# Kernel optimization log

Measured on AMD Instinct MI355X. Metric: run time of the kernel, lower is better.

Reference implementation:

```python
import jax, jax.numpy as jnp
import numpy as np

GRAPH_ALPHA = 3.0
HOP_ALPHA = 0.05
TOP_K = 30


def conv1x1(x, W, b):
    # x: [B,C,N,T], W: [O,C] -> [B,O,N,T]
    return jnp.einsum('bcnt,oc->bont', x, W) + b[None, :, None, None]


def tconv(x, W, b):
    # temporal conv along T, kernel (1,3), 'same' padding. W: [O,I,1,3]
    y = jax.lax.conv_general_dilated(x, W, (1, 1), ((0, 0), (1, 1)),
                                     dimension_numbers=('NCHW', 'OIHW', 'NCHW'))
    return y + b[None, :, None, None]


def mixprop(x, adj, W, b):
    # 1-hop mix-prop graph diffusion (gcn_depth=1, hopalpha=0.05)
    n = adj.shape[0]
    A = adj + jnp.eye(n, dtype=adj.dtype)
    A = A / A.sum(axis=1, keepdims=True)
    h = HOP_ALPHA * x + (1.0 - HOP_ALPHA) * jnp.einsum('bcvt,vw->bcwt', x, A)
    return conv1x1(jnp.concatenate([x, h], axis=1), W, b)


def st_block(x, adj, tf_w, tf_b, tg_w, tg_b, g1_w, g1_b, g2_w, g2_b,
             end_w, end_b, out_w, out_b):
    h = jnp.tanh(tconv(x, tf_w, tf_b)) * jax.nn.sigmoid(tconv(x, tg_w, tg_b))
    h = mixprop(h, adj, g1_w, g1_b) + mixprop(h, adj.T, g2_w, g2_b)
    h = jax.nn.relu(conv1x1(h, end_w, end_b))
    return conv1x1(h, out_w, out_b)


def build_adj(idx, emb1, emb2, l1_w, l1_b, l2_w, l2_b):
    e1, e2 = emb1[idx], emb2[idx]
    n1 = jnp.tanh(GRAPH_ALPHA * (e1 @ l1_w.T + l1_b))
    n2 = jnp.tanh(GRAPH_ALPHA * (e2 @ l2_w.T + l2_b))
    a = n1 @ n2.T - n2 @ n1.T
    adj = jax.nn.relu(jnp.tanh(GRAPH_ALPHA * a))
    _, top_idx = jax.lax.top_k(adj, TOP_K)
    rows = jnp.arange(adj.shape[0])[:, None]
    mask = jnp.zeros_like(adj).at[rows, top_idx].set(1.0)
    return adj * mask


def setup_inputs() -> dict:
    B, T, N, D = 16, 128, 1024, 64
    ks = jax.random.split(jax.random.key(0), 24)
    def w(i, shape):
        return jax.random.normal(ks[i], shape, dtype=jnp.float32) * 0.1
    z = lambda *s: jnp.zeros(s, jnp.float32)
    return {
        'x': jax.random.normal(ks[0], (B, T, N), dtype=jnp.float32),
        'idx': jnp.arange(N, dtype=jnp.int32),
        'emb1': w(1, (N, D)), 'emb2': w(2, (N, D)),
        'lin1_w': w(3, (D, D)), 'lin1_b': z(D),
        'lin2_w': w(4, (D, D)), 'lin2_b': z(D),
        'w_start': w(5, (16, 1)), 'b_start': z(16),
        'enc_tf_w': w(6, (16, 16, 1, 3)), 'enc_tf_b': z(16),
        'enc_tg_w': w(7, (16, 16, 1, 3)), 'enc_tg_b': z(16),
        'enc_g1_w': w(8, (16, 32)), 'enc_g1_b': z(16),
        'enc_g2_w': w(9, (16, 32)), 'enc_g2_b': z(16),
        'enc_end_w': w(10, (32, 16)), 'enc_end_b': z(32),
        'enc_out_w': w(11, (64, 32)), 'enc_out_b': z(64),
        'dec_tf_w': w(12, (64, 64, 1, 3)), 'dec_tf_b': z(64),
        'dec_tg_w': w(13, (64, 64, 1, 3)), 'dec_tg_b': z(64),
        'dec_g1_w': w(14, (64, 128)), 'dec_g1_b': z(64),
        'dec_g2_w': w(15, (64, 128)), 'dec_g2_b': z(64),
        'dec_end_w': w(16, (32, 64)), 'dec_end_b': z(32),
        'dec_out_w': w(17, (16, 32)), 'dec_out_b': z(16),
        'w_end': w(18, (1, 16)), 'b_end': z(1),
    }


def reference(x, idx, emb1, emb2, lin1_w, lin1_b, lin2_w, lin2_b,
              w_start, b_start,
              enc_tf_w, enc_tf_b, enc_tg_w, enc_tg_b, enc_g1_w, enc_g1_b,
              enc_g2_w, enc_g2_b, enc_end_w, enc_end_b, enc_out_w, enc_out_b,
              dec_tf_w, dec_tf_b, dec_tg_w, dec_tg_b, dec_g1_w, dec_g1_b,
              dec_g2_w, dec_g2_b, dec_end_w, dec_end_b, dec_out_w, dec_out_b,
              w_end, b_end):
    adj = build_adj(idx, emb1, emb2, lin1_w, lin1_b, lin2_w, lin2_b)
    h = jnp.transpose(x, (0, 2, 1))[:, None]  # [B,1,N,T]
    h = conv1x1(h, w_start, b_start)          # [B,16,N,T]
    z = st_block(h, adj, enc_tf_w, enc_tf_b, enc_tg_w, enc_tg_b,
                 enc_g1_w, enc_g1_b, enc_g2_w, enc_g2_b,
                 enc_end_w, enc_end_b, enc_out_w, enc_out_b)  # [B,64,N,T]
    y = st_block(z, adj, dec_tf_w, dec_tf_b, dec_tg_w, dec_tg_b,
                 dec_g1_w, dec_g1_b, dec_g2_w, dec_g2_b,
                 dec_end_w, dec_end_b, dec_out_w, dec_out_b)  # [B,16,N,T]
    y = conv1x1(y, w_end, b_end)               # [B,1,N,T]
    return jnp.transpose(y[:, 0], (0, 2, 1))   # [B,T,N]
```

## Files before the change

### kernel.cpp

```cpp
#include <hip/hip_runtime.h>
#include <math.h>

#define NN   1024
#define TTL  128
#define NTP  131072
#define TOPK 30

#define OEGTF_T 0
#define OEGTF_C 48
#define OEGTF_B 96
#define OEGTG_T 112
#define OEGTG_C 160
#define OEGTG_B 208
#define OEE0    224
#define OEE1    736
#define OEE2    1248
#define OEEB    1760
#define OEOUT_W 1792
#define OEOUT_B 3840
#define ODTF_B  16192
#define ODTG_B  28544
#define ODEB    34752
#define OWC     34784
#define OBC     34816
#define ODEALL  59456
#define ODTW2   65600
#define OCF     77888
#define OCG     78080
#define WTOT    78272


__global__ void k_prep_weights(
    const float* __restrict__ w_start, const float* __restrict__ b_start,
    const float* __restrict__ etf_w, const float* __restrict__ etf_b,
    const float* __restrict__ etg_w, const float* __restrict__ etg_b,
    const float* __restrict__ eg1_w, const float* __restrict__ eg1_b,
    const float* __restrict__ eg2_w, const float* __restrict__ eg2_b,
    const float* __restrict__ eend_w, const float* __restrict__ eend_b,
    const float* __restrict__ eout_w, const float* __restrict__ eout_b,
    const float* __restrict__ dtf_w, const float* __restrict__ dtf_b,
    const float* __restrict__ dtg_w, const float* __restrict__ dtg_b,
    const float* __restrict__ dg1_w, const float* __restrict__ dg1_b,
    const float* __restrict__ dg2_w, const float* __restrict__ dg2_b,
    const float* __restrict__ dend_w, const float* __restrict__ dend_b,
    const float* __restrict__ dout_w, const float* __restrict__ dout_b,
    const float* __restrict__ w_end, const float* __restrict__ b_end,
    float* __restrict__ W)
{
    int tid = blockIdx.x*blockDim.x + threadIdx.x;
    int nthr = gridDim.x*blockDim.x;
    for (int id=tid; id<96; id+=nthr){
        int which = id/48; int r = id%48; int o = r/3, k = r%3;
        const float* w = which ? etg_w : etf_w;
        double t=0.0, c=0.0;
        for (int i=0;i<16;i++){
            double wv = (double)w[(o*16+i)*3+k];
            t += wv*(double)w_start[i];
            c += wv*(double)b_start[i];
        }
        W[(which?OEGTG_T:OEGTF_T)+o*3+k] = (float)t;
        W[(which?OEGTG_C:OEGTF_C)+o*3+k] = (float)c;
    }
    for (int i=tid;i<16;i+=nthr){
        W[OEGTF_B+i] = etf_b[i];
        W[OEGTG_B+i] = etg_b[i];
    }
    for (int id=tid; id<512; id+=nthr){
        int i = id>>5, o2 = id&31;
        double s0=0.0, s1=0.0, s2=0.0;
        for (int o=0;o<16;o++){
            double m0 = (double)eg1_w[o*32+i] + (double)eg2_w[o*32+i]
                      + 0.05*((double)eg1_w[o*32+16+i] + (double)eg2_w[o*32+16+i]);
            double m1 = 0.95*(double)eg1_w[o*32+16+i];
            double m2 = 0.95*(double)eg2_w[o*32+16+i];
            double ew = (double)eend_w[o2*16+o];
            s0 += ew*m0; s1 += ew*m1; s2 += ew*m2;
        }
        W[OEE0+i*32+o2]=(float)s0; W[OEE1+i*32+o2]=(float)s1; W[OEE2+i*32+o2]=(float)s2;
    }
    for (int o2=tid; o2<32; o2+=nthr){
        double s = (double)eend_b[o2];
        for (int o=0;o<16;o++) s += (double)eend_w[o2*16+o]*((double)eg1_b[o]+(double)eg2_b[o]);
        W[OEEB+o2] = (float)s;
    }
    for (int i=tid;i<64;i+=nthr){
        W[ODTF_B+i]=dtf_b[i]; W[ODTG_B+i]=dtg_b[i];
    }
    for (int id=tid; id<12288; id+=nthr){
        int oc = id/3072; int rem = id%3072; int j = rem/96; int q = rem%96;
        const float* w = (q<48) ? dtf_w : dtg_w;
        int q2 = (q<48) ? q : q-48;
        int o = q2/3, k = q2%3;
        double s = 0.0;
        for (int i=0;i<64;i++)
            s += (double)w[((oc*16+o)*64+i)*3+k]*(double)eout_w[i*32+j];
        W[ODTW2+id] = (float)s;
    }
    for (int id=tid; id<384; id+=nthr){
        int which = id/192; int r = id%192;
        int oc = r/48; int q = r%48; int o = q/3, k = q%3;
        const float* w = which ? dtg_w : dtf_w;
        double s = 0.0;
        for (int i=0;i<64;i++)
            s += (double)w[((oc*16+o)*64+i)*3+k]*(double)eout_b[i];
        W[(which?OCG:OCF) + oc*48 + o*3 + k] = (float)s;
    }
    for (int id=tid; id<6144; id+=nthr){
        int i = id/96, j = id%96;
        double s = 0.0;
        if (j < 32){
            int o2 = j;
            for (int o=0;o<64;o++){
                double m1 = 0.95*(double)dg1_w[o*128+64+i];
                s += (double)dend_w[o2*64+o]*m1;
            }
        } else if (j < 64){
            int o2 = j-32;
            for (int o=0;o<64;o++){
                double m2 = 0.95*(double)dg2_w[o*128+64+i];
                s += (double)dend_w[o2*64+o]*m2;
            }
        } else {
            int o2 = j-64;
            for (int o=0;o<64;o++){
                double m0 = (double)dg1_w[o*128+i] + (double)dg2_w[o*128+i]
                          + 0.05*((double)dg1_w[o*128+64+i] + (double)dg2_w[o*128+64+i]);
                s += (double)dend_w[o2*64+o]*m0;
            }
        }
        W[ODEALL+id] = (float)s;
    }
    for (int o2=tid; o2<32; o2+=nthr){
        double s = (double)dend_b[o2];
        for (int o=0;o<64;o++) s += (double)dend_w[o2*64+o]*((double)dg1_b[o]+(double)dg2_b[o]);
        W[ODEB+o2] = (float)s;
        double wc = 0.0;
        for (int o3=0;o3<16;o3++) wc += (double)w_end[o3]*(double)dout_w[o3*32+o2];
        W[OWC+o2] = (float)wc;
    }
    if (tid==0){
        double bc = (double)b_end[0];
        for (int o3=0;o3<16;o3++) bc += (double)w_end[o3]*(double)dout_b[o3];
        W[OBC] = (float)bc;
    }
}

__global__ void k_emb(const int* __restrict__ idxp,
                      const float* __restrict__ emb1, const float* __restrict__ emb2,
                      const float* __restrict__ l1w, const float* __restrict__ l1b,
                      const float* __restrict__ l2w, const float* __restrict__ l2b,
                      double* __restrict__ n1, double* __restrict__ n2)
{
    int id = blockIdx.x*blockDim.x + threadIdx.x;
    int i = id>>6, d = id&63;
    int ii = idxp[i];
    double a1 = (double)l1b[d], a2 = (double)l2b[d];
    for (int k=0;k<64;k++){
        a1 += (double)emb1[ii*64+k]*(double)l1w[d*64+k];
        a2 += (double)emb2[ii*64+k]*(double)l2w[d*64+k];
    }
    n1[id] = tanh(3.0*a1);
    n2[id] = tanh(3.0*a2);
}

__global__ __launch_bounds__(64) void k_topk(
    const double* __restrict__ n1, const double* __restrict__ n2,
    int* __restrict__ topc, double* __restrict__ topv,
    double* __restrict__ rs1, double* __restrict__ colsum)
{
    __shared__ double arow[NN];
    __shared__ double sn1[64], sn2[64];
    int i = blockIdx.x, lane = threadIdx.x;
    sn1[lane] = n1[i*64+lane];
    sn2[lane] = n2[i*64+lane];
    __syncthreads();
    for (int jb=0;jb<16;jb++){
        int j = jb*64 + lane;
        const double* p2 = n2 + (long)j*64;
        const double* p1 = n1 + (long)j*64;
        double d1v=0.0, d2v=0.0;
        for (int d=0;d<64;d++){ d1v += sn1[d]*p2[d]; d2v += sn2[d]*p1[d]; }
        double a = tanh(3.0*(d1v - d2v));
        arow[j] = a>0.0 ? a : 0.0;
    }
    __syncthreads();
    double lv = -2.0; int lj = 1<<30;
    for (int jb=0;jb<16;jb++){
        int j = jb*64+lane;
        double v = arow[j];
        if (v>lv || (v==lv && j<lj)){ lv=v; lj=j; }
    }
    double rsum = 0.0;
    for (int r=0;r<TOPK;r++){
        double bv = lv; int bj = lj;
        for (int off=32; off>=1; off>>=1){
            double ov = __shfl_xor(bv, off, 64);
            int    oj = __shfl_xor(bj, off, 64);
            if (ov>bv || (ov==bv && oj<bj)){ bv=ov; bj=oj; }
        }
        if (lane == (bj & 63)){
            arow[bj] = -2.0;
            lv = -2.0; lj = 1<<30;
            for (int jb=0;jb<16;jb++){
                int j = jb*64+lane;
                double v = arow[j];
                if (v>lv || (v==lv && j<lj)){ lv=v; lj=j; }
            }
        }
        if (lane == 0){
            topc[i*TOPK+r] = bj;
            topv[i*TOPK+r] = bv;
            if (bv > 0.0) atomicAdd(&colsum[bj], bv);
        }
        rsum += (bv > 0.0 ? bv : 0.0);
    }
    if (lane == 0) rs1[i] = 1.0 + rsum;
}

__global__ void k_csc(const int* __restrict__ topc, const double* __restrict__ topv,
                      const double* __restrict__ rs1,
                      int* __restrict__ ccount, int* __restrict__ cidx, float* __restrict__ cw)
{
    int w = blockIdx.x*blockDim.x + threadIdx.x;
    if (w >= NN) return;
    double rv = rs1[w];
    for (int r=0;r<TOPK;r++){
        double v = topv[w*TOPK+r];
        if (v > 0.0){
            int col = topc[w*TOPK+r];
            int pos = atomicAdd(&ccount[col], 1);
            cidx[(long)col*NN+pos] = w;
            cw  [(long)col*NN+pos] = (float)(v / rv);
        }
    }
}

__global__ void k_pad(int* __restrict__ ccount, int* __restrict__ cidx, float* __restrict__ cw)
{
    int col = blockIdx.x*blockDim.x + threadIdx.x;
    if (col >= NN) return;
    int cnt = ccount[col];
    int padded = (cnt + 7) & ~7;
    for (int e = cnt; e < padded; e++){
        cidx[(long)col*NN + e] = 0;
        cw  [(long)col*NN + e] = 0.0f;
    }
    ccount[col] = padded;
}

__global__ void k_post1(const double* __restrict__ colsum, const double* __restrict__ rs1,
                        double* __restrict__ rs2, float* __restrict__ d1, float* __restrict__ d2)
{
    int v = blockIdx.x*blockDim.x + threadIdx.x;
    if (v >= NN) return;
    double r2 = 1.0 + colsum[v];
    rs2[v] = r2;
    d2[v] = (float)(1.0/r2);
    d1[v] = (float)(1.0/rs1[v]);
}

__global__ void k_post2(const int* __restrict__ topc, const double* __restrict__ topv,
                        const double* __restrict__ rs2,
                        int* __restrict__ topc2, float* __restrict__ ew2b)
{
    int e = blockIdx.x*blockDim.x + threadIdx.x;
    if (e >= NN*32) return;
    int w = e>>5, r = e&31;
    if (r < TOPK){
        double v = topv[w*TOPK+r];
        int c = topc[w*TOPK+r];
        topc2[e] = (v > 0.0) ? c : 0;
        ew2b[e]  = (v > 0.0) ? (float)(v / rs2[c]) : 0.0f;
    } else {
        topc2[e] = 0;
        ew2b[e]  = 0.0f;
    }
}


__global__ __launch_bounds__(256) void k_enc_gg(const float* __restrict__ x,
    float* __restrict__ eg, float* __restrict__ es1, float* __restrict__ es2,
    const float* __restrict__ Wt,
    const int* __restrict__ ccount, const int* __restrict__ cidx, const float* __restrict__ cw,
    const int* __restrict__ topc2, const float* __restrict__ ew2b,
    const float* __restrict__ d1, const float* __restrict__ d2,
    long S, int b0)
{
    __shared__ float4 lA[NN];
    __shared__ float4 lB[NN];
    int tid = threadIdx.x, c = blockIdx.y, cb = blockIdx.z, t0 = blockIdx.x*8;
    float ft[3], fc[3], gt[3], gcc[3];
    #pragma unroll
    for (int k=0;k<3;k++){
        ft[k]=Wt[OEGTF_T+c*3+k]; fc[k]=Wt[OEGTF_C+c*3+k];
        gt[k]=Wt[OEGTG_T+c*3+k]; gcc[k]=Wt[OEGTG_C+c*3+k];
    }
    float fb = Wt[OEGTF_B+c], gb = Wt[OEGTG_B+c];
    const float* xb = x + (long)(b0+cb)*NTP + (long)t0*NN;
    long base = (long)c*S + (long)cb*NTP + (long)t0*NN;
    bool hl0 = (t0>0), hr7 = (t0+8<TTL);
    for (int q=0;q<4;q++){
        int v = q*256 + tid;
        float xr[10];
        xr[0] = hl0 ? xb[v-NN] : 0.0f;
        #pragma unroll
        for (int k=0;k<8;k++) xr[k+1] = xb[v+(long)k*NN];
        xr[9] = hr7 ? xb[v+(long)8*NN] : 0.0f;
        float gg[8];
        #pragma unroll
        for (int k=0;k<8;k++){
            float atf = fb + ft[1]*xr[k+1] + fc[1];
            float atg = gb + gt[1]*xr[k+1] + gcc[1];
            bool hL = (k>0) || hl0;
            bool hR = (k<7) || hr7;
            if (hL){ atf += ft[0]*xr[k] + fc[0]; atg += gt[0]*xr[k] + gcc[0]; }
            if (hR){ atf += ft[2]*xr[k+2] + fc[2]; atg += gt[2]*xr[k+2] + gcc[2]; }
            gg[k] = tanhf(atf)/(1.0f+expf(-atg));
            eg[base + (long)k*NN + v] = gg[k];
        }
        lA[v] = make_float4(gg[0],gg[1],gg[2],gg[3]);
        lB[v] = make_float4(gg[4],gg[5],gg[6],gg[7]);
    }
    __syncthreads();
    for (int wb=0;wb<4;wb++){
        int w = wb*256 + tid;
        float4 ga = lA[w], gbv = lB[w];
        float dv = d1[w];
        float a0=ga.x*dv, a1=ga.y*dv, a2=ga.z*dv, a3=ga.w*dv;
        float a4=gbv.x*dv, a5=gbv.y*dv, a6=gbv.z*dv, a7=gbv.w*dv;
        int cnt = ccount[w];
        const int4*   ci4 = (const int4*)  (cidx + (long)w*NN);
        const float4* cw4 = (const float4*)(cw   + (long)w*NN);
        for (int e=0; e<cnt; e+=4){
            int4 ia = ci4[e>>2];
            float4 wa = cw4[e>>2];
            float4 s, u;
            s = lA[ia.x]; u = lB[ia.x];
            a0 += wa.x*s.x; a1 += wa.x*s.y; a2 += wa.x*s.z; a3 += wa.x*s.w;
            a4 += wa.x*u.x; a5 += wa.x*u.y; a6 += wa.x*u.z; a7 += wa.x*u.w;
            s = lA[ia.y]; u = lB[ia.y];
            a0 += wa.y*s.x; a1 += wa.y*s.y; a2 += wa.y*s.z; a3 += wa.y*s.w;
            a4 += wa.y*u.x; a5 += wa.y*u.y; a6 += wa.y*u.z; a7 += wa.y*u.w;
            s = lA[ia.z]; u = lB[ia.z];
            a0 += wa.z*s.x; a1 += wa.z*s.y; a2 += wa.z*s.z; a3 += wa.z*s.w;
            a4 += wa.z*u.x; a5 += wa.z*u.y; a6 += wa.z*u.z; a7 += wa.z*u.w;
            s = lA[ia.w]; u = lB[ia.w];
            a0 += wa.w*s.x; a1 += wa.w*s.y; a2 += wa.w*s.z; a3 += wa.w*s.w;
            a4 += wa.w*u.x; a5 += wa.w*u.y; a6 += wa.w*u.z; a7 += wa.w*u.w;
        }
        es1[base+w]=a0; es1[base+NN+w]=a1; es1[base+2*NN+w]=a2; es1[base+3*NN+w]=a3;
        es1[base+4*NN+w]=a4; es1[base+5*NN+w]=a5; es1[base+6*NN+w]=a6; es1[base+7*NN+w]=a7;
        float dw = d2[w];
        a0=ga.x*dw; a1=ga.y*dw; a2=ga.z*dw; a3=ga.w*dw;
        a4=gbv.x*dw; a5=gbv.y*dw; a6=gbv.z*dw; a7=gbv.w*dw;
        const int4*   tc4 = (const int4*)  (topc2 + w*32);
        const float4* e24 = (const float4*)(ew2b  + w*32);
        #pragma unroll
        for (int r=0;r<8;r++){
            int4 ic = tc4[r]; float4 wv = e24[r];
            float4 s, u;
            s = lA[ic.x]; u = lB[ic.x];
            a0 += wv.x*s.x; a1 += wv.x*s.y; a2 += wv.x*s.z; a3 += wv.x*s.w;
            a4 += wv.x*u.x; a5 += wv.x*u.y; a6 += wv.x*u.z; a7 += wv.x*u.w;
            s = lA[ic.y]; u = lB[ic.y];
            a0 += wv.y*s.x; a1 += wv.y*s.y; a2 += wv.y*s.z; a3 += wv.y*s.w;
            a4 += wv.y*u.x; a5 += wv.y*u.y; a6 += wv.y*u.z; a7 += wv.y*u.w;
            s = lA[ic.z]; u = lB[ic.z];
            a0 += wv.z*s.x; a1 += wv.z*s.y; a2 += wv.z*s.z; a3 += wv.z*s.w;
            a4 += wv.z*u.x; a5 += wv.z*u.y; a6 += wv.z*u.z; a7 += wv.z*u.w;
            s = lA[ic.w]; u = lB[ic.w];
            a0 += wv.w*s.x; a1 += wv.w*s.y; a2 += wv.w*s.z; a3 += wv.w*s.w;
            a4 += wv.w*u.x; a5 += wv.w*u.y; a6 += wv.w*u.z; a7 += wv.w*u.w;
        }
        es2[base+w]=a0; es2[base+NN+w]=a1; es2[base+2*NN+w]=a2; es2[base+3*NN+w]=a3;
        es2[base+4*NN+w]=a4; es2[base+5*NN+w]=a5; es2[base+6*NN+w]=a6; es2[base+7*NN+w]=a7;
    }
}

__global__ __launch_bounds__(256) void k_enc_tail(const float* __restrict__ Bp,
    float* __restrict__ E32, const float* __restrict__ Wt, long S)
{
    long p = (long)blockIdx.x*256 + threadIdx.x;
    float e[32];
    #pragma unroll
    for (int o2=0;o2<32;o2++) e[o2] = Wt[OEEB+o2];
    for (int i=0;i<16;i++){
        float a = Bp[(long)i*S+p], b = Bp[(long)(16+i)*S+p], c = Bp[(long)(32+i)*S+p];
        const float* w0 = Wt+OEE0+i*32;
        const float* w1 = Wt+OEE1+i*32;
        const float* w2 = Wt+OEE2+i*32;
        #pragma unroll
        for (int o2=0;o2<32;o2++) e[o2] += w0[o2]*a + w1[o2]*b + w2[o2]*c;
    }
    #pragma unroll
    for (int o2=0;o2<32;o2++){
        float v = e[o2];
        E32[(long)o2*S+p] = v>0.0f ? v : 0.0f;
    }
}

__global__ __launch_bounds__(256) void k_dec_gate(const float* __restrict__ E32,
    float* __restrict__ g, const float* __restrict__ Wt, long S)
{
    int oc = blockIdx.y;
    long pos = (long)blockIdx.x*256 + threadIdx.x;
    int t = (int)((pos>>10) & (TTL-1));
    bool hasL = (t>0), hasR = (t<TTL-1);
    float af[16], ag[16];
    #pragma unroll
    for (int o=0;o<16;o++){
        float bf = Wt[ODTF_B+oc*16+o] + Wt[OCF+oc*48+o*3+1];
        float bg = Wt[ODTG_B+oc*16+o] + Wt[OCG+oc*48+o*3+1];
        if (hasL){ bf += Wt[OCF+oc*48+o*3];   bg += Wt[OCG+oc*48+o*3]; }
        if (hasR){ bf += Wt[OCF+oc*48+o*3+2]; bg += Wt[OCG+oc*48+o*3+2]; }
        af[o]=bf; ag[o]=bg;
    }
    #pragma unroll 1
    for (int j=0;j<32;j++){
        const float* xp = E32 + (long)j*S + pos;
        float xc = xp[0];
        float xl = hasL ? xp[-NN] : 0.0f;
        float xr = hasR ? xp[NN]  : 0.0f;
        const float* wfg = Wt + ODTW2 + (long)(oc*32+j)*96;
        #pragma unroll
        for (int o=0;o<16;o++){
            af[o] += wfg[o*3]*xl + wfg[o*3+1]*xc + wfg[o*3+2]*xr;
            ag[o] += wfg[48+o*3]*xl + wfg[48+o*3+1]*xc + wfg[48+o*3+2]*xr;
        }
    }
    #pragma unroll
    for (int o=0;o<16;o++){
        g[(long)(oc*16+o)*S + pos] = tanhf(af[o])/(1.0f+expf(-ag[o]));
    }
}

__global__ __launch_bounds__(256) void k_dec_conv(const float* __restrict__ g,
    float* __restrict__ Cp, float* __restrict__ P0p,
    const float* __restrict__ Wt, long S)
{
    long p = (long)blockIdx.x*256 + threadIdx.x;
    int jc = blockIdx.y;
    if (jc == 0){
        float a1[32], a2[32];
        #pragma unroll
        for (int jj=0;jj<32;jj++){ a1[jj]=0.0f; a2[jj]=0.0f; }
        #pragma unroll 1
        for (int i=0;i<64;i++){
            float gv = g[(long)i*S+p];
            const float* wr = Wt + ODEALL + i*96;
            #pragma unroll
            for (int jj=0;jj<32;jj++){ a1[jj] += wr[jj]*gv; a2[jj] += wr[32+jj]*gv; }
        }
        #pragma unroll
        for (int jj=0;jj<32;jj++){
            Cp[(long)jj*S+p] = a1[jj];
            Cp[(long)(32+jj)*S+p] = a2[jj];
        }
    } else {
        float a0[32];
        #pragma unroll
        for (int jj=0;jj<32;jj++) a0[jj] = Wt[ODEB+jj];
        #pragma unroll 1
        for (int i=0;i<64;i++){
            float gv = g[(long)i*S+p];
            const float* wr = Wt + ODEALL + i*96 + 64;
            #pragma unroll
            for (int jj=0;jj<32;jj++) a0[jj] += wr[jj]*gv;
        }
        #pragma unroll
        for (int jj=0;jj<32;jj++) P0p[(long)jj*S+p] = a0[jj];
    }
}

__global__ __launch_bounds__(256) void k_graph32f(const float* __restrict__ P1,
    const float* __restrict__ P2, const float* __restrict__ P0,
    float* __restrict__ part,
    const int* __restrict__ ccount, const int* __restrict__ cidx, const float* __restrict__ cw,
    const int* __restrict__ topc2, const float* __restrict__ ew2b,
    const float* __restrict__ d1, const float* __restrict__ d2,
    const float* __restrict__ Wt, long S)
{
    __shared__ float4 lA[NN];
    __shared__ float4 lB[NN];
    int tid = threadIdx.x;
    int grp = blockIdx.y, cb = blockIdx.z, t0 = blockIdx.x*8;
    long tbase = (long)cb*NTP + (long)t0*NN;
    float res[4][8];
    #pragma unroll
    for (int wb=0;wb<4;wb++){
        #pragma unroll
        for (int k=0;k<8;k++) res[wb][k]=0.0f;
    }
    float q1[4][8];
    for (int c4=0;c4<4;c4++){
        int ch = grp*4 + c4;
        long base = (long)ch*S + tbase;
        if (c4) __syncthreads();
        const float* s1 = P1 + base;
        for (int q=0;q<4;q++){
            int v = q*256 + tid;
            lA[v] = make_float4(s1[v], s1[v+NN], s1[v+2*NN], s1[v+3*NN]);
            lB[v] = make_float4(s1[v+4*NN], s1[v+5*NN], s1[v+6*NN], s1[v+7*NN]);
        }
        __syncthreads();
        for (int wb=0;wb<4;wb++){
            int w = wb*256 + tid;
            float4 ga = lA[w], gbv = lB[w];
            float dv = d1[w];
            float a0=ga.x*dv, a1=ga.y*dv, a2=ga.z*dv, a3=ga.w*dv;
            float a4=gbv.x*dv, a5=gbv.y*dv, a6=gbv.z*dv, a7=gbv.w*dv;
            int cnt = ccount[w];
            const int4*   ci4 = (const int4*)  (cidx + (long)w*NN);
            const float4* cw4 = (const float4*)(cw   + (long)w*NN);
            for (int e=0; e<cnt; e+=4){
                int4 ia = ci4[e>>2];
                float4 wa = cw4[e>>2];
                float4 s, u;
                s = lA[ia.x]; u = lB[ia.x];
                a0 += wa.x*s.x; a1 += wa.x*s.y; a2 += wa.x*s.z; a3 += wa.x*s.w;
                a4 += wa.x*u.x; a5 += wa.x*u.y; a6 += wa.x*u.z; a7 += wa.x*u.w;
                s = lA[ia.y]; u = lB[ia.y];
                a0 += wa.y*s.x; a1 += wa.y*s.y; a2 += wa.y*s.z; a3 += wa.y*s.w;
                a4 += wa.y*u.x; a5 += wa.y*u.y; a6 += wa.y*u.z; a7 += wa.y*u.w;
                s = lA[ia.z]; u = lB[ia.z];
                a0 += wa.z*s.x; a1 += wa.z*s.y; a2 += wa.z*s.z; a3 += wa.z*s.w;
                a4 += wa.z*u.x; a5 += wa.z*u.y; a6 += wa.z*u.z; a7 += wa.z*u.w;
                s = lA[ia.w]; u = lB[ia.w];
                a0 += wa.w*s.x; a1 += wa.w*s.y; a2 += wa.w*s.z; a3 += wa.w*s.w;
                a4 += wa.w*u.x; a5 += wa.w*u.y; a6 += wa.w*u.z; a7 += wa.w*u.w;
            }
            q1[wb][0]=a0; q1[wb][1]=a1; q1[wb][2]=a2; q1[wb][3]=a3;
            q1[wb][4]=a4; q1[wb][5]=a5; q1[wb][6]=a6; q1[wb][7]=a7;
        }
        __syncthreads();
        const float* s2 = P2 + base;
        for (int q=0;q<4;q++){
            int v = q*256 + tid;
            lA[v] = make_float4(s2[v], s2[v+NN], s2[v+2*NN], s2[v+3*NN]);
            lB[v] = make_float4(s2[v+4*NN], s2[v+5*NN], s2[v+6*NN], s2[v+7*NN]);
        }
        __syncthreads();
        float wc = Wt[OWC+ch];
        const float* p0 = P0 + base;
        for (int wb=0;wb<4;wb++){
            int w = wb*256 + tid;
            float4 ga = lA[w], gbv = lB[w];
            float dw = d2[w];
            float a0=ga.x*dw, a1=ga.y*dw, a2=ga.z*dw, a3=ga.w*dw;
            float a4=gbv.x*dw, a5=gbv.y*dw, a6=gbv.z*dw, a7=gbv.w*dw;
            const int4*   tc4 = (const int4*)  (topc2 + w*32);
            const float4* e24 = (const float4*)(ew2b  + w*32);
            #pragma unroll
            for (int r=0;r<8;r++){
                int4 ic = tc4[r]; float4 wv = e24[r];
                float4 s, u;
                s = lA[ic.x]; u = lB[ic.x];
                a0 += wv.x*s.x; a1 += wv.x*s.y; a2 += wv.x*s.z; a3 += wv.x*s.w;
                a4 += wv.x*u.x; a5 += wv.x*u.y; a6 += wv.x*u.z; a7 += wv.x*u.w;
                s = lA[ic.y]; u = lB[ic.y];
                a0 += wv.y*s.x; a1 += wv.y*s.y; a2 += wv.y*s.z; a3 += wv.y*s.w;
                a4 += wv.y*u.x; a5 += wv.y*u.y; a6 += wv.y*u.z; a7 += wv.y*u.w;
                s = lA[ic.z]; u = lB[ic.z];
                a0 += wv.z*s.x; a1 += wv.z*s.y; a2 += wv.z*s.z; a3 += wv.z*s.w;
                a4 += wv.z*u.x; a5 += wv.z*u.y; a6 += wv.z*u.z; a7 += wv.z*u.w;
                s = lA[ic.w]; u = lB[ic.w];
                a0 += wv.w*s.x; a1 += wv.w*s.y; a2 += wv.w*s.z; a3 += wv.w*s.w;
                a4 += wv.w*u.x; a5 += wv.w*u.y; a6 += wv.w*u.z; a7 += wv.w*u.w;
            }
            float e0,e1,e2,e3,e4,e5,e6,e7;
            e0 = p0[w]      + q1[wb][0] + a0;
            e1 = p0[NN+w]   + q1[wb][1] + a1;
            e2 = p0[2*NN+w] + q1[wb][2] + a2;
            e3 = p0[3*NN+w] + q1[wb][3] + a3;
            e4 = p0[4*NN+w] + q1[wb][4] + a4;
            e5 = p0[5*NN+w] + q1[wb][5] + a5;
            e6 = p0[6*NN+w] + q1[wb][6] + a6;
            e7 = p0[7*NN+w] + q1[wb][7] + a7;
            e0 = e0>0.0f?e0:0.0f; e1 = e1>0.0f?e1:0.0f;
            e2 = e2>0.0f?e2:0.0f; e3 = e3>0.0f?e3:0.0f;
            e4 = e4>0.0f?e4:0.0f; e5 = e5>0.0f?e5:0.0f;
            e6 = e6>0.0f?e6:0.0f; e7 = e7>0.0f?e7:0.0f;
            res[wb][0] += wc*e0; res[wb][1] += wc*e1;
            res[wb][2] += wc*e2; res[wb][3] += wc*e3;
            res[wb][4] += wc*e4; res[wb][5] += wc*e5;
            res[wb][6] += wc*e6; res[wb][7] += wc*e7;
        }
    }
    long pb = (long)grp*S + tbase;
    for (int wb=0;wb<4;wb++){
        int w = wb*256 + tid;
        #pragma unroll
        for (int k=0;k<8;k++) part[pb+(long)k*NN+w] = res[wb][k];
    }
}

__global__ __launch_bounds__(256) void k_comb(const float* __restrict__ part,
    const float* __restrict__ Wt, float* __restrict__ out, long S, int b0)
{
    long p = (long)blockIdx.x*256 + threadIdx.x;
    float r = Wt[OBC];
    #pragma unroll
    for (int gp=0; gp<8; gp++) r += part[(long)gp*S+p];
    out[(long)b0*NTP + p] = r;
}


extern "C" void kernel_launch(void* const* d_in, const int* in_sizes, int n_in,
                              void* d_out, int out_size, void* d_ws, size_t ws_size,
                              hipStream_t stream)
{
    const float* x      = (const float*)d_in[0];
    const int*   idx    = (const int*)  d_in[1];
    const float* emb1   = (const float*)d_in[2];
    const float* emb2   = (const float*)d_in[3];
    const float* lin1_w = (const float*)d_in[4];
    const float* lin1_b = (const float*)d_in[5];
    const float* lin2_w = (const float*)d_in[6];
    const float* lin2_b = (const float*)d_in[7];
    const float* w_start= (const float*)d_in[8];
    const float* b_start= (const float*)d_in[9];
    const float* etf_w  = (const float*)d_in[10];
    const float* etf_b  = (const float*)d_in[11];
    const float* etg_w  = (const float*)d_in[12];
    const float* etg_b  = (const float*)d_in[13];
    const float* eg1_w  = (const float*)d_in[14];
    const float* eg1_b  = (const float*)d_in[15];
    const float* eg2_w  = (const float*)d_in[16];
    const float* eg2_b  = (const float*)d_in[17];
    const float* eend_w = (const float*)d_in[18];
    const float* eend_b = (const float*)d_in[19];
    const float* eout_w = (const float*)d_in[20];
    const float* eout_b = (const float*)d_in[21];
    const float* dtf_w  = (const float*)d_in[22];
    const float* dtf_b  = (const float*)d_in[23];
    const float* dtg_w  = (const float*)d_in[24];
    const float* dtg_b  = (const float*)d_in[25];
    const float* dg1_w  = (const float*)d_in[26];
    const float* dg1_b  = (const float*)d_in[27];
    const float* dg2_w  = (const float*)d_in[28];
    const float* dg2_b  = (const float*)d_in[29];
    const float* dend_w = (const float*)d_in[30];
    const float* dend_b = (const float*)d_in[31];
    const float* dout_w = (const float*)d_in[32];
    const float* dout_b = (const float*)d_in[33];
    const float* w_end  = (const float*)d_in[34];
    const float* b_end  = (const float*)d_in[35];
    float* out = (float*)d_out;

    char* basep = (char*)d_ws;
    size_t cur = 0;
    auto alloc = [&](size_t bytes)->void* {
        void* p = basep + cur;
        cur = (cur + bytes + 511) & ~(size_t)511;
        return p;
    };
    float*  W     = (float*) alloc(WTOT*sizeof(float));
    double* n1    = (double*)alloc(65536*sizeof(double));
    double* n2    = (double*)alloc(65536*sizeof(double));
    double* topv  = (double*)alloc((size_t)NN*TOPK*sizeof(double));
    int*    topc  = (int*)   alloc((size_t)NN*TOPK*sizeof(int));
    double* rs1   = (double*)alloc(NN*sizeof(double));
    double* rs2   = (double*)alloc(NN*sizeof(double));
    double* colsum= (double*)alloc(NN*sizeof(double));
    float*  d1a   = (float*) alloc(NN*sizeof(float));
    float*  d2a   = (float*) alloc(NN*sizeof(float));
    int*    topc2 = (int*)   alloc((size_t)NN*32*sizeof(int));
    float*  ew2b  = (float*) alloc((size_t)NN*32*sizeof(float));
    int*    ccount= (int*)   alloc(NN*sizeof(int));
    int*    cidx  = (int*)   alloc((size_t)NN*NN*sizeof(int));
    float*  cw    = (float*) alloc((size_t)NN*NN*sizeof(float));

    size_t perb = (size_t)176 * NTP * sizeof(float);
    int CB = 1;
    for (int c = 16; c >= 1; c >>= 1){
        if (cur + perb*(size_t)c <= ws_size){ CB = c; break; }
    }
    long S = (long)CB * NTP;
    float* A = (float*)alloc((size_t)64*S*sizeof(float));
    float* B = (float*)alloc((size_t)48*S*sizeof(float));
    float* C = (float*)alloc((size_t)64*S*sizeof(float));

    (void)hipMemsetAsync(colsum, 0, NN*sizeof(double), stream);
    (void)hipMemsetAsync(ccount, 0, NN*sizeof(int), stream);

    k_prep_weights<<<32,256,0,stream>>>(
        w_start,b_start, etf_w,etf_b, etg_w,etg_b, eg1_w,eg1_b, eg2_w,eg2_b,
        eend_w,eend_b, eout_w,eout_b, dtf_w,dtf_b, dtg_w,dtg_b, dg1_w,dg1_b,
        dg2_w,dg2_b, dend_w,dend_b, dout_w,dout_b, w_end,b_end, W);
    k_emb<<<256,256,0,stream>>>(idx, emb1, emb2, lin1_w, lin1_b, lin2_w, lin2_b, n1, n2);
    k_topk<<<NN,64,0,stream>>>(n1, n2, topc, topv, rs1, colsum);
    k_csc<<<4,256,0,stream>>>(topc, topv, rs1, ccount, cidx, cw);
    k_pad<<<4,256,0,stream>>>(ccount, cidx, cw);
    k_post1<<<4,256,0,stream>>>(colsum, rs1, rs2, d1a, d2a);
    k_post2<<<(NN*32+255)/256,256,0,stream>>>(topc, topv, rs2, topc2, ew2b);

    int nch = 16 / CB;
    for (int ch=0; ch<nch; ch++){
        int b0 = ch*CB;
        k_enc_gg<<<dim3(16,16,CB),256,0,stream>>>(x, B, B+(long)16*S, B+(long)32*S, W,
            ccount,cidx,cw, topc2,ew2b, d1a,d2a, S, b0);
        k_enc_tail<<<512*CB,256,0,stream>>>(B, A, W, S);
        k_dec_gate<<<dim3(512*CB,4),256,0,stream>>>(A, C, W, S);
        k_dec_conv<<<dim3(512*CB,2),256,0,stream>>>(C, A, B, W, S);
        k_graph32f<<<dim3(16,8,CB),256,0,stream>>>(A, A+(long)32*S, B, C,
            ccount,cidx,cw, topc2,ew2b, d1a,d2a, W, S);
        k_comb<<<512*CB,256,0,stream>>>(C, W, out, S, b0);
    }
    (void)in_sizes; (void)n_in; (void)out_size;
}
```

Before: 3.625 ms.

## Fuse decoder gate and conv kernels via LDS; transpose embeddings for top-k

Merges the decoder gated temporal conv and the following 1x1 projection kernels into one kernel. The 64-channel gate output now stays in a 64KB shared-memory tile instead of round-tripping through global memory, and buffer roles are reshuffled to match. Separately, the embedding kernel also writes transposed copies of n1/n2 so the top-k dot products read coalesced columns. The trade-off is less parallelism, since each block now does all four gate output groups serially, and the large LDS footprint limits occupancy.

```diff
diff --git a/kernel.cpp b/kernel.cpp
--- a/kernel.cpp
+++ b/kernel.cpp
@@ -149,7 +149,8 @@
                       const float* __restrict__ emb1, const float* __restrict__ emb2,
                       const float* __restrict__ l1w, const float* __restrict__ l1b,
                       const float* __restrict__ l2w, const float* __restrict__ l2b,
-                      double* __restrict__ n1, double* __restrict__ n2)
+                      double* __restrict__ n1, double* __restrict__ n2,
+                      double* __restrict__ n1T, double* __restrict__ n2T)
 {
     int id = blockIdx.x*blockDim.x + threadIdx.x;
     int i = id>>6, d = id&63;
@@ -159,12 +160,14 @@
         a1 += (double)emb1[ii*64+k]*(double)l1w[d*64+k];
         a2 += (double)emb2[ii*64+k]*(double)l2w[d*64+k];
     }
-    n1[id] = tanh(3.0*a1);
-    n2[id] = tanh(3.0*a2);
+    double v1 = tanh(3.0*a1), v2 = tanh(3.0*a2);
+    n1[id] = v1;            n2[id] = v2;
+    n1T[d*NN+i] = v1;       n2T[d*NN+i] = v2;
 }
 
 __global__ __launch_bounds__(64) void k_topk(
     const double* __restrict__ n1, const double* __restrict__ n2,
+    const double* __restrict__ n1T, const double* __restrict__ n2T,
     int* __restrict__ topc, double* __restrict__ topv,
     double* __restrict__ rs1, double* __restrict__ colsum)
 {
@@ -176,10 +179,11 @@
     __syncthreads();
     for (int jb=0;jb<16;jb++){
         int j = jb*64 + lane;
-        const double* p2 = n2 + (long)j*64;
-        const double* p1 = n1 + (long)j*64;
         double d1v=0.0, d2v=0.0;
-        for (int d=0;d<64;d++){ d1v += sn1[d]*p2[d]; d2v += sn2[d]*p1[d]; }
+        for (int d=0;d<64;d++){
+            d1v += sn1[d]*n2T[d*NN+j];
+            d2v += sn2[d]*n1T[d*NN+j];
+        }
         double a = tanh(3.0*(d1v - d2v));
         arow[j] = a>0.0 ? a : 0.0;
     }
@@ -399,70 +403,66 @@
     }
 }
 
-__global__ __launch_bounds__(256) void k_dec_gate(const float* __restrict__ E32,
-    float* __restrict__ g, const float* __restrict__ Wt, long S)
-{
-    int oc = blockIdx.y;
-    long pos = (long)blockIdx.x*256 + threadIdx.x;
-    int t = (int)((pos>>10) & (TTL-1));
+__global__ __launch_bounds__(256) void k_dec_fused(const float* __restrict__ E32,
+    float* __restrict__ P12, float* __restrict__ P0p,
+    const float* __restrict__ Wt, long S)
+{
+    __shared__ float gl[64*256];
+    int tid = threadIdx.x;
+    long p = (long)blockIdx.x*256 + tid;
+    int t = (int)((p>>10) & (TTL-1));
     bool hasL = (t>0), hasR = (t<TTL-1);
-    float af[16], ag[16];
-    #pragma unroll
-    for (int o=0;o<16;o++){
-        float bf = Wt[ODTF_B+oc*16+o] + Wt[OCF+oc*48+o*3+1];
-        float bg = Wt[ODTG_B+oc*16+o] + Wt[OCG+oc*48+o*3+1];
-        if (hasL){ bf += Wt[OCF+oc*48+o*3];   bg += Wt[OCG+oc*48+o*3]; }
-        if (hasR){ bf += Wt[OCF+oc*48+o*3+2]; bg += Wt[OCG+oc*48+o*3+2]; }
-        af[o]=bf; ag[o]=bg;
-    }
-    #pragma unroll 1
-    for (int j=0;j<32;j++){
-        const float* xp = E32 + (long)j*S + pos;
-        float xc = xp[0];
-        float xl = hasL ? xp[-NN] : 0.0f;
-        float xr = hasR ? xp[NN]  : 0.0f;
-        const float* wfg = Wt + ODTW2 + (long)(oc*32+j)*96;
+    for (int oc=0; oc<4; oc++){
+        float af[16], ag[16];
         #pragma unroll
         for (int o=0;o<16;o++){
-            af[o] += wfg[o*3]*xl + wfg[o*3+1]*xc + wfg[o*3+2]*xr;
-            ag[o] += wfg[48+o*3]*xl + wfg[48+o*3+1]*xc + wfg[48+o*3+2]*xr;
-        }
-    }
-    #pragma unroll
-    for (int o=0;o<16;o++){
-        g[(long)(oc*16+o)*S + pos] = tanhf(af[o])/(1.0f+expf(-ag[o]));
-    }
-}
-
-__global__ __launch_bounds__(256) void k_dec_conv(const float* __restrict__ g,
-    float* __restrict__ Cp, float* __restrict__ P0p,
-    const float* __restrict__ Wt, long S)
-{
-    long p = (long)blockIdx.x*256 + threadIdx.x;
-    int jc = blockIdx.y;
-    if (jc == 0){
+            float bf = Wt[ODTF_B+oc*16+o] + Wt[OCF+oc*48+o*3+1];
+            float bg = Wt[ODTG_B+oc*16+o] + Wt[OCG+oc*48+o*3+1];
+            if (hasL){ bf += Wt[OCF+oc*48+o*3];   bg += Wt[OCG+oc*48+o*3]; }
+            if (hasR){ bf += Wt[OCF+oc*48+o*3+2]; bg += Wt[OCG+oc*48+o*3+2]; }
+            af[o]=bf; ag[o]=bg;
+        }
+        #pragma unroll 1
+        for (int j=0;j<32;j++){
+            const float* xp = E32 + (long)j*S + p;
+            float xc = xp[0];
+            float xl = hasL ? xp[-NN] : 0.0f;
+            float xr = hasR ? xp[NN]  : 0.0f;
+            const float* wfg = Wt + ODTW2 + (long)(oc*32+j)*96;
+            #pragma unroll
+            for (int o=0;o<16;o++){
+                af[o] += wfg[o*3]*xl + wfg[o*3+1]*xc + wfg[o*3+2]*xr;
+                ag[o] += wfg[48+o*3]*xl + wfg[48+o*3+1]*xc + wfg[48+o*3+2]*xr;
+            }
+        }
+        #pragma unroll
+        for (int o=0;o<16;o++)
+            gl[(oc*16+o)*256 + tid] = tanhf(af[o])/(1.0f+expf(-ag[o]));
+    }
+    {
         float a1[32], a2[32];
         #pragma unroll
         for (int jj=0;jj<32;jj++){ a1[jj]=0.0f; a2[jj]=0.0f; }
         #pragma unroll 1
         for (int i=0;i<64;i++){
-            float gv = g[(long)i*S+p];
+            float gv = gl[i*256 + tid];
             const float* wr = Wt + ODEALL + i*96;
             #pragma unroll
             for (int jj=0;jj<32;jj++){ a1[jj] += wr[jj]*gv; a2[jj] += wr[32+jj]*gv; }
         }
         #pragma unroll
         for (int jj=0;jj<32;jj++){
-            Cp[(long)jj*S+p] = a1[jj];
-            Cp[(long)(32+jj)*S+p] = a2[jj];
-        }
-    } else {
+            P12[(long)jj*S+p] = a1[jj];
+            P12[(long)(32+jj)*S+p] = a2[jj];
+        }
+    }
+    {
         float a0[32];
         #pragma unroll
         for (int jj=0;jj<32;jj++) a0[jj] = Wt[ODEB+jj];
         #pragma unroll 1
         for (int i=0;i<64;i++){
-            float gv = g[(long)i*S+p];
+            float gv = gl[i*256 + tid];
             const float* wr = Wt + ODEALL + i*96 + 64;
             #pragma unroll
             for (int jj=0;jj<32;jj++) a0[jj] += wr[jj]*gv;
@@ -657,6 +657,8 @@
     float*  W     = (float*) alloc(WTOT*sizeof(float));
     double* n1    = (double*)alloc(65536*sizeof(double));
     double* n2    = (double*)alloc(65536*sizeof(double));
+    double* n1T   = (double*)alloc(65536*sizeof(double));
+    double* n2T   = (double*)alloc(65536*sizeof(double));
     double* topv  = (double*)alloc((size_t)NN*TOPK*sizeof(double));
     int*    topc  = (int*)   alloc((size_t)NN*TOPK*sizeof(int));
     double* rs1   = (double*)alloc(NN*sizeof(double));
@@ -687,8 +689,9 @@
         w_start,b_start, etf_w,etf_b, etg_w,etg_b, eg1_w,eg1_b, eg2_w,eg2_b,
         eend_w,eend_b, eout_w,eout_b, dtf_w,dtf_b, dtg_w,dtg_b, dg1_w,dg1_b,
         dg2_w,dg2_b, dend_w,dend_b, dout_w,dout_b, w_end,b_end, W);
-    k_emb<<<256,256,0,stream>>>(idx, emb1, emb2, lin1_w, lin1_b, lin2_w, lin2_b, n1, n2);
-    k_topk<<<NN,64,0,stream>>>(n1, n2, topc, topv, rs1, colsum);
+    k_emb<<<256,256,0,stream>>>(idx, emb1, emb2, lin1_w, lin1_b, lin2_w, lin2_b,
+                                n1, n2, n1T, n2T);
+    k_topk<<<NN,64,0,stream>>>(n1, n2, n1T, n2T, topc, topv, rs1, colsum);
     k_csc<<<4,256,0,stream>>>(topc, topv, rs1, ccount, cidx, cw);
     k_pad<<<4,256,0,stream>>>(ccount, cidx, cw);
     k_post1<<<4,256,0,stream>>>(colsum, rs1, rs2, d1a, d2a);
@@ -700,11 +703,10 @@
         k_enc_gg<<<dim3(16,16,CB),256,0,stream>>>(x, B, B+(long)16*S, B+(long)32*S, W,
             ccount,cidx,cw, topc2,ew2b, d1a,d2a, S, b0);
         k_enc_tail<<<512*CB,256,0,stream>>>(B, A, W, S);
-        k_dec_gate<<<dim3(512*CB,4),256,0,stream>>>(A, C, W, S);
-        k_dec_conv<<<dim3(512*CB,2),256,0,stream>>>(C, A, B, W, S);
-        k_graph32f<<<dim3(16,8,CB),256,0,stream>>>(A, A+(long)32*S, B, C,
+        k_dec_fused<<<512*CB,256,0,stream>>>(A, C, B, W, S);
+        k_graph32f<<<dim3(16,8,CB),256,0,stream>>>(C, C+(long)32*S, B, A,
             ccount,cidx,cw, topc2,ew2b, d1a,d2a, W, S);
-        k_comb<<<512*CB,256,0,stream>>>(C, W, out, S, b0);
+        k_comb<<<512*CB,256,0,stream>>>(A, W, out, S, b0);
     }
     (void)in_sizes; (void)n_in; (void)out_size;
 }
```

Result: slower. 5.376 ms (+48.3%).

## Split adjacency dot products from top-k scan and interleave decoder block indices

Applied to the files above, without the earlier changes.

The combined top-k kernel, which ran 64-thread blocks over a full adjacency row, is split in two. A 256-thread dot-product kernel writes the dense fp64 adjacency to a new 8 MB workspace buffer, and a separate 64-lane scan kernel reads each row back for top-k selection. The goal is more parallelism in the dot products, at the cost of an extra global round trip. The decoder gate and conv kernels also flatten their 2D grids so that neighbouring blocks share a position tile across output-channel groups, which should improve cache reuse of the input.

```diff
diff --git a/kernel.cpp b/kernel.cpp
--- a/kernel.cpp
+++ b/kernel.cpp
@@ -163,26 +163,36 @@
     n2[id] = tanh(3.0*a2);
 }
 
-__global__ __launch_bounds__(64) void k_topk(
+__global__ __launch_bounds__(256) void k_dots(
     const double* __restrict__ n1, const double* __restrict__ n2,
-    int* __restrict__ topc, double* __restrict__ topv,
-    double* __restrict__ rs1, double* __restrict__ colsum)
-{
-    __shared__ double arow[NN];
+    double* __restrict__ AA)
+{
     __shared__ double sn1[64], sn2[64];
-    int i = blockIdx.x, lane = threadIdx.x;
-    sn1[lane] = n1[i*64+lane];
-    sn2[lane] = n2[i*64+lane];
+    int i = blockIdx.x, tid = threadIdx.x;
+    if (tid < 64){ sn1[tid] = n1[i*64+tid]; sn2[tid] = n2[i*64+tid]; }
     __syncthreads();
-    for (int jb=0;jb<16;jb++){
-        int j = jb*64 + lane;
+    double* rowp = AA + (long)i*NN;
+    #pragma unroll
+    for (int q=0;q<4;q++){
+        int j = q*256 + tid;
         const double* p2 = n2 + (long)j*64;
         const double* p1 = n1 + (long)j*64;
         double d1v=0.0, d2v=0.0;
         for (int d=0;d<64;d++){ d1v += sn1[d]*p2[d]; d2v += sn2[d]*p1[d]; }
         double a = tanh(3.0*(d1v - d2v));
-        arow[j] = a>0.0 ? a : 0.0;
-    }
+        rowp[j] = a>0.0 ? a : 0.0;
+    }
+}
+
+__global__ __launch_bounds__(64) void k_scan(
+    const double* __restrict__ AA,
+    int* __restrict__ topc, double* __restrict__ topv,
+    double* __restrict__ rs1, double* __restrict__ colsum)
+{
+    __shared__ double arow[NN];
+    int i = blockIdx.x, lane = threadIdx.x;
+    const double* src = AA + (long)i*NN;
+    for (int jb=0;jb<16;jb++) arow[jb*64+lane] = src[jb*64+lane];
     __syncthreads();
     double lv = -2.0; int lj = 1<<30;
     for (int jb=0;jb<16;jb++){
@@ -402,8 +412,9 @@
 __global__ __launch_bounds__(256) void k_dec_gate(const float* __restrict__ E32,
     float* __restrict__ g, const float* __restrict__ Wt, long S)
 {
-    int oc = blockIdx.y;
-    long pos = (long)blockIdx.x*256 + threadIdx.x;
+    int bx = blockIdx.x;
+    int oc = bx & 3;
+    long pos = (long)(bx >> 2)*256 + threadIdx.x;
     int t = (int)((pos>>10) & (TTL-1));
     bool hasL = (t>0), hasR = (t<TTL-1);
     float af[16], ag[16];
@@ -438,8 +449,9 @@
     float* __restrict__ Cp, float* __restrict__ P0p,
     const float* __restrict__ Wt, long S)
 {
-    long p = (long)blockIdx.x*256 + threadIdx.x;
-    int jc = blockIdx.y;
+    int bx = blockIdx.x;
+    int jc = bx & 1;
+    long p = (long)(bx >> 1)*256 + threadIdx.x;
     if (jc == 0){
         float a1[32], a2[32];
         #pragma unroll
@@ -657,6 +669,7 @@
     float*  W     = (float*) alloc(WTOT*sizeof(float));
     double* n1    = (double*)alloc(65536*sizeof(double));
     double* n2    = (double*)alloc(65536*sizeof(double));
+    double* AA    = (double*)alloc((size_t)NN*NN*sizeof(double));
     double* topv  = (double*)alloc((size_t)NN*TOPK*sizeof(double));
     int*    topc  = (int*)   alloc((size_t)NN*TOPK*sizeof(int));
     double* rs1   = (double*)alloc(NN*sizeof(double));
@@ -688,7 +701,8 @@
         eend_w,eend_b, eout_w,eout_b, dtf_w,dtf_b, dtg_w,dtg_b, dg1_w,dg1_b,
         dg2_w,dg2_b, dend_w,dend_b, dout_w,dout_b, w_end,b_end, W);
     k_emb<<<256,256,0,stream>>>(idx, emb1, emb2, lin1_w, lin1_b, lin2_w, lin2_b, n1, n2);
-    k_topk<<<NN,64,0,stream>>>(n1, n2, topc, topv, rs1, colsum);
+    k_dots<<<NN,256,0,stream>>>(n1, n2, AA);
+    k_scan<<<NN,64,0,stream>>>(AA, topc, topv, rs1, colsum);
     k_csc<<<4,256,0,stream>>>(topc, topv, rs1, ccount, cidx, cw);
     k_pad<<<4,256,0,stream>>>(ccount, cidx, cw);
     k_post1<<<4,256,0,stream>>>(colsum, rs1, rs2, d1a, d2a);
@@ -700,8 +714,8 @@
         k_enc_gg<<<dim3(16,16,CB),256,0,stream>>>(x, B, B+(long)16*S, B+(long)32*S, W,
             ccount,cidx,cw, topc2,ew2b, d1a,d2a, S, b0);
         k_enc_tail<<<512*CB,256,0,stream>>>(B, A, W, S);
-        k_dec_gate<<<dim3(512*CB,4),256,0,stream>>>(A, C, W, S);
-        k_dec_conv<<<dim3(512*CB,2),256,0,stream>>>(C, A, B, W, S);
+        k_dec_gate<<<2048*CB,256,0,stream>>>(A, C, W, S);
+        k_dec_conv<<<1024*CB,256,0,stream>>>(C, A, B, W, S);
         k_graph32f<<<dim3(16,8,CB),256,0,stream>>>(A, A+(long)32*S, B, C,
             ccount,cidx,cw, topc2,ew2b, d1a,d2a, W, S);
         k_comb<<<512*CB,256,0,stream>>>(C, W, out, S, b0);
```

New measurement: 3.723 ms. 1.03x slower.
